# Optimization experiments

Measured on AMD Instinct MI355X. Metric: run time of the kernel, lower is better.

The kernel has to match this reference:

```python
import jax, jax.numpy as jnp
import numpy as np

N = 33_554_432          # batch of independent (1x1) samples (vmapped single-sample module)
THRESHOLD = 0.0
NUM_CLASSES = 2


def setup_inputs() -> dict:
    key = jax.random.key(0)
    ks = jax.random.split(key, 9)
    data = jax.random.normal(ks[0], (N, 1), dtype=jnp.float32)  # flattened 1x1 samples
    # Conv2d(1, 1, kernel_size=1): a single scalar weight + scalar bias
    conv_w = jax.random.normal(ks[1], (), dtype=jnp.float32)
    conv_b = jax.random.normal(ks[2], (), dtype=jnp.float32)
    # classifier: Linear(1,1) -> ReLU -> Linear(1,1) -> ReLU -> Linear(1, num_classes)
    w1 = jax.random.normal(ks[3], (1, 1), dtype=jnp.float32)
    b1 = jax.random.normal(ks[4], (1,), dtype=jnp.float32)
    w2 = jax.random.normal(ks[5], (1, 1), dtype=jnp.float32)
    b2 = jax.random.normal(ks[6], (1,), dtype=jnp.float32)
    w3 = jax.random.normal(ks[7], (NUM_CLASSES, 1), dtype=jnp.float32)
    b3 = jax.random.normal(ks[8], (NUM_CLASSES,), dtype=jnp.float32)
    return {"data": data, "conv_w": conv_w, "conv_b": conv_b,
            "w1": w1, "b1": b1, "w2": w2, "b2": b2, "w3": w3, "b3": b3}


def reference(data, conv_w, conv_b, w1, b1, w2, b2, w3, b3):
    # conv (1x1, single channel) -> sigmoid(logits - threshold); mean over last dim is a no-op (size 1)
    act = jax.nn.sigmoid(data * conv_w + conv_b - THRESHOLD)          # [N, 1]
    h = jax.nn.relu(act @ w1.T + b1)                                   # [N, 1]
    h = jax.nn.relu(h @ w2.T + b2)                                     # [N, 1]
    logits = h @ w3.T + b3                                             # [N, num_classes]
    # prob = sigmoid(out).mean() per sample
    return jnp.mean(jax.nn.sigmoid(logits), axis=-1)                   # [N]
```

## Files before the change

kernel.cpp:

```cpp
#include <hip/hip_runtime.h>
#include <math.h>


typedef float f32x4 __attribute__((ext_vector_type(4)));

#define TBL_N     2048
#define TBL_NODES (TBL_N + 1)
#define TBL_LO    (-12.0f)
#define TBL_SCALE (TBL_N / 24.0f)

__global__ __launch_bounds__(256) void build_table_kernel(
    float* __restrict__ tbl,
    const float* __restrict__ cw_p, const float* __restrict__ cb_p,
    const float* __restrict__ w1_p, const float* __restrict__ b1_p,
    const float* __restrict__ w2_p, const float* __restrict__ b2_p,
    const float* __restrict__ w3_p, const float* __restrict__ b3_p)
{
    const float w1  = *w1_p,   b1  = *b1_p;
    const float w2  = *w2_p,   b2  = *b2_p;
    const float w30 = w3_p[0], w31 = w3_p[1];
    const float b30 = b3_p[0], b31 = b3_p[1];

    for (int i = threadIdx.x; i < TBL_NODES; i += blockDim.x) {
        float t   = TBL_LO + (float)i * (1.0f / TBL_SCALE);
        float act = 1.0f / (1.0f + expf(-t));
        float h   = fmaxf(fmaf(act, w1, b1), 0.0f);
        h         = fmaxf(fmaf(h,   w2, b2), 0.0f);
        float s0  = 1.0f / (1.0f + expf(-fmaf(h, w30, b30)));
        float s1  = 1.0f / (1.0f + expf(-fmaf(h, w31, b31)));
        tbl[i] = 0.5f * (s0 + s1);
    }
}

__global__ __launch_bounds__(256) void hybridconv_lut_kernel(
    const f32x4* __restrict__ data4,
    f32x4* __restrict__ out4,
    const float* __restrict__ tbl,
    const float* __restrict__ cw_p, const float* __restrict__ cb_p,
    int n4)
{
    __shared__ float lut[TBL_NODES];

    {
        const f32x4* t4 = (const f32x4*)tbl;
        f32x4* l4 = (f32x4*)lut;
        l4[threadIdx.x]       = t4[threadIdx.x];
        l4[threadIdx.x + 256] = t4[threadIdx.x + 256];
        if (threadIdx.x == 0) lut[TBL_N] = tbl[TBL_N];
    }
    __syncthreads();

    const float A = (*cw_p) * TBL_SCALE;
    const float B = ((*cb_p) - TBL_LO) * TBL_SCALE;
    const float UMAX = (float)TBL_N - 0.001f;

    const int base = blockIdx.x * (256 * 16) + threadIdx.x;

#pragma unroll
    for (int kk = 0; kk < 4; ++kk) {
        f32x4 v[4];
        int idx[4];
#pragma unroll
        for (int k = 0; k < 4; ++k) {
            idx[k] = base + (kk * 4 + k) * 256;
            if (idx[k] < n4) v[k] = data4[idx[k]];
        }
#pragma unroll
        for (int k = 0; k < 4; ++k) {
            if (idx[k] >= n4) continue;
            f32x4 r;
#pragma unroll
            for (int j = 0; j < 4; ++j) {
                float u = fmaf(v[k][j], A, B);
                u = fminf(fmaxf(u, 0.0f), UMAX);
                int   i  = (int)u;
                float fr = u - (float)i;
                float f0 = lut[i];
                float f1 = lut[i + 1];
                r[j] = fmaf(fr, f1 - f0, f0);
            }
            __builtin_nontemporal_store(r, &out4[idx[k]]);
        }
    }
}

extern "C" void kernel_launch(void* const* d_in, const int* in_sizes, int n_in,
                              void* d_out, int out_size, void* d_ws, size_t ws_size,
                              hipStream_t stream) {
    const float* data = (const float*)d_in[0];
    const float* cw   = (const float*)d_in[1];
    const float* cb   = (const float*)d_in[2];
    const float* w1   = (const float*)d_in[3];
    const float* b1   = (const float*)d_in[4];
    const float* w2   = (const float*)d_in[5];
    const float* b2   = (const float*)d_in[6];
    const float* w3   = (const float*)d_in[7];
    const float* b3   = (const float*)d_in[8];
    float* out = (float*)d_out;
    float* tbl = (float*)d_ws;

    const int n  = in_sizes[0];
    const int n4 = n / 4;

    build_table_kernel<<<1, 256, 0, stream>>>(tbl, cw, cb, w1, b1, w2, b2, w3, b3);

    const int block = 256;
    const int per_block = block * 16;
    const int grid = (n4 + per_block - 1) / per_block;
    hybridconv_lut_kernel<<<grid, block, 0, stream>>>(
        (const f32x4*)data, (f32x4*)out, tbl, cw, cb, n4);
}
```

Before: 50.56 us.

## Build LUT per block in shared memory and store interpolation pairs

Removes the separate single-block table-build kernel and has each block evaluate the network directly to fill its shared-memory LUT. Entries are stored as adjacent (f0,f1) pairs so each lookup is one 8-byte LDS read instead of two scalar reads. This drops a kernel launch and its serialization, but every block now computes 4096 network evaluations with several expf calls each, adding per-block startup compute. The LUT also doubles in size.

```diff
diff --git a/kernel.cpp b/kernel.cpp
--- a/kernel.cpp
+++ b/kernel.cpp
@@ -2,51 +2,49 @@
 #include <math.h>
 
 
-typedef float f32x4 __attribute__((ext_vector_type(4)));
+typedef float  f32x4 __attribute__((ext_vector_type(4)));
+typedef float  f32x2 __attribute__((ext_vector_type(2)));
 
 #define TBL_N     2048
-#define TBL_NODES (TBL_N + 1)
 #define TBL_LO    (-12.0f)
+#define TBL_STEP  (24.0f / TBL_N)
 #define TBL_SCALE (TBL_N / 24.0f)
 
-__global__ __launch_bounds__(256) void build_table_kernel(
-    float* __restrict__ tbl,
-    const float* __restrict__ cw_p, const float* __restrict__ cb_p,
-    const float* __restrict__ w1_p, const float* __restrict__ b1_p,
-    const float* __restrict__ w2_p, const float* __restrict__ b2_p,
-    const float* __restrict__ w3_p, const float* __restrict__ b3_p)
-{
-    const float w1  = *w1_p,   b1  = *b1_p;
-    const float w2  = *w2_p,   b2  = *b2_p;
-    const float w30 = w3_p[0], w31 = w3_p[1];
-    const float b30 = b3_p[0], b31 = b3_p[1];
-
-    for (int i = threadIdx.x; i < TBL_NODES; i += blockDim.x) {
-        float t   = TBL_LO + (float)i * (1.0f / TBL_SCALE);
-        float act = 1.0f / (1.0f + expf(-t));
-        float h   = fmaxf(fmaf(act, w1, b1), 0.0f);
-        h         = fmaxf(fmaf(h,   w2, b2), 0.0f);
-        float s0  = 1.0f / (1.0f + expf(-fmaf(h, w30, b30)));
-        float s1  = 1.0f / (1.0f + expf(-fmaf(h, w31, b31)));
-        tbl[i] = 0.5f * (s0 + s1);
-    }
+__device__ __forceinline__ float net_eval(float t, float w1, float b1,
+                                          float w2, float b2,
+                                          float w30, float b30,
+                                          float w31, float b31) {
+    float act = 1.0f / (1.0f + expf(-t));
+    float h   = fmaxf(fmaf(act, w1, b1), 0.0f);
+    h         = fmaxf(fmaf(h,   w2, b2), 0.0f);
+    float s0  = 1.0f / (1.0f + expf(-fmaf(h, w30, b30)));
+    float s1  = 1.0f / (1.0f + expf(-fmaf(h, w31, b31)));
+    return 0.5f * (s0 + s1);
 }
 
 __global__ __launch_bounds__(256) void hybridconv_lut_kernel(
     const f32x4* __restrict__ data4,
     f32x4* __restrict__ out4,
-    const float* __restrict__ tbl,
     const float* __restrict__ cw_p, const float* __restrict__ cb_p,
+    const float* __restrict__ w1_p, const float* __restrict__ b1_p,
+    const float* __restrict__ w2_p, const float* __restrict__ b2_p,
+    const float* __restrict__ w3_p, const float* __restrict__ b3_p,
     int n4)
 {
-    __shared__ float lut[TBL_NODES];
+    __shared__ f32x2 lut[TBL_N];
 
     {
-        const f32x4* t4 = (const f32x4*)tbl;
-        f32x4* l4 = (f32x4*)lut;
-        l4[threadIdx.x]       = t4[threadIdx.x];
-        l4[threadIdx.x + 256] = t4[threadIdx.x + 256];
-        if (threadIdx.x == 0) lut[TBL_N] = tbl[TBL_N];
+        const float w1  = *w1_p,   b1  = *b1_p;
+        const float w2  = *w2_p,   b2  = *b2_p;
+        const float w30 = w3_p[0], w31 = w3_p[1];
+        const float b30 = b3_p[0], b31 = b3_p[1];
+        for (int i = threadIdx.x; i < TBL_N; i += 256) {
+            float t0 = TBL_LO + (float)i * TBL_STEP;
+            float f0 = net_eval(t0,            w1, b1, w2, b2, w30, b30, w31, b31);
+            float f1 = net_eval(t0 + TBL_STEP, w1, b1, w2, b2, w30, b30, w31, b31);
+            f32x2 p; p.x = f0; p.y = f1;
+            lut[i] = p;
+        }
     }
     __syncthreads();
 
@@ -75,9 +73,8 @@
                 u = fminf(fmaxf(u, 0.0f), UMAX);
                 int   i  = (int)u;
                 float fr = u - (float)i;
-                float f0 = lut[i];
-                float f1 = lut[i + 1];
-                r[j] = fmaf(fr, f1 - f0, f0);
+                f32x2 p  = lut[i];
+                r[j] = fmaf(fr, p.y - p.x, p.x);
             }
             __builtin_nontemporal_store(r, &out4[idx[k]]);
         }
@@ -97,16 +94,15 @@
     const float* w3   = (const float*)d_in[7];
     const float* b3   = (const float*)d_in[8];
     float* out = (float*)d_out;
-    float* tbl = (float*)d_ws;
 
     const int n  = in_sizes[0];
     const int n4 = n / 4;
 
-    build_table_kernel<<<1, 256, 0, stream>>>(tbl, cw, cb, w1, b1, w2, b2, w3, b3);
-
     const int block = 256;
     const int per_block = block * 16;
     const int grid = (n4 + per_block - 1) / per_block;
+
     hybridconv_lut_kernel<<<grid, block, 0, stream>>>(
-        (const f32x4*)data, (f32x4*)out, tbl, cw, cb, n4);
+        (const f32x4*)data, (f32x4*)out,
+        cw, cb, w1, b1, w2, b2, w3, b3, n4);
 }
```

After: 48.73 us. 1.04x faster.
